# Performance work log

Hardware: AMD Instinct MI355X
Metric: run time of the kernel (lower is better)

Reference implementation:

```python
import jax, jax.numpy as jnp
import numpy as np

B, C, H, W = 4, 256, 128, 256
NUM_CODES = 256  # codebook rows; dim_code == C


def setup_inputs() -> dict:
    key = jax.random.key(0)
    k_feat, k_code = jax.random.split(key)
    feature = jax.random.normal(k_feat, (B, C, H, W), dtype=jnp.float32)
    codebook = jax.random.normal(k_code, (NUM_CODES, C), dtype=jnp.float32)
    return {"feature": feature, "codebook": codebook}


def reference(feature, codebook):
    # Faithful to ComminPub.sender core:
    #   weights = (feature_expand * codebooks).sum(dim=2) / (codebooks*codebooks).sum(dim=2)
    # expressed as a contraction over C instead of materializing [B,N,C,H,W].
    code_norm = jnp.sum(codebook * codebook, axis=1)          # [N]
    weights = jnp.einsum('bchw,nc->bnhw', feature, codebook)   # [B,N,H,W]
    weights = weights / code_norm[None, :, None, None]
    # fc_after_rbdc reconstruction: einsum('b n h w, n c -> b c h w', weights, codebook)
    recon = jnp.einsum('bnhw,nc->bchw', weights, codebook)     # [B,C,H,W]
    return recon
```

## Files before the change

### kernel.cpp

```cpp
#include <hip/hip_runtime.h>
#include <hip/hip_bf16.h>
#include <cstdint>

#define CDIM   256
#define NCODES 256
#define HWB    32768
#define BATCH  4
#define BN     64
#define BK     32

typedef __bf16 bf16x8 __attribute__((ext_vector_type(8)));
typedef float  f32x4  __attribute__((ext_vector_type(4)));

__global__ void norms_kernel(const float* __restrict__ cb, float* __restrict__ inv_norm) {
    const int n = blockIdx.x;
    const int lane = threadIdx.x;
    const float* row = cb + n * CDIM;
    float s = 0.f;
#pragma unroll
    for (int c = 0; c < CDIM; c += 64) {
        float v = row[c + lane];
        s += v * v;
    }
#pragma unroll
    for (int off = 32; off > 0; off >>= 1) s += __shfl_down(s, off, 64);
    if (lane == 0) inv_norm[n] = 1.0f / s;
}

__global__ void mmat_kernel(const float* __restrict__ cb, const float* __restrict__ inv_norm,
                            __bf16* __restrict__ Mb) {
    const int i = blockIdx.x;
    const int j = threadIdx.x;
    float acc = 0.f;
#pragma unroll 4
    for (int n = 0; n < NCODES; ++n) {
        acc += (cb[n * CDIM + i] * inv_norm[n]) * cb[n * CDIM + j];
    }
    Mb[i * CDIM + j] = (__bf16)acc;
}

__global__ __launch_bounds__(256, 4) void recon_kernel(
    const float* __restrict__ feat, const __bf16* __restrict__ Mb,
    float* __restrict__ out) {
    __shared__ __align__(16) __bf16 Alds[CDIM * BK];
    __shared__ __align__(16) __bf16 Blds[BN * BK];

    const int tid  = threadIdx.x;
    const int lane = tid & 63;
    const int w    = tid >> 6;
    const int quad = lane >> 4;
    const int l16  = lane & 15;

    const int b  = blockIdx.y;
    const int p0 = blockIdx.x * BN;

    const float* fbase = feat + ((size_t)b * CDIM) * HWB + p0;
    float*       obase = out  + ((size_t)b * CDIM) * HWB + p0;

    f32x4 acc[4][4];
#pragma unroll
    for (int mt = 0; mt < 4; ++mt)
#pragma unroll
        for (int nt = 0; nt < 4; ++nt)
            acc[mt][nt] = (f32x4){0.f, 0.f, 0.f, 0.f};

    const float* fp = fbase + (size_t)(w * 8) * HWB + lane;

    for (int kc = 0; kc < 8; ++kc) {
        float fv[8];
#pragma unroll
        for (int j = 0; j < 8; ++j)
            fv[j] = fp[(size_t)j * HWB];

#pragma unroll
        for (int j = 0; j < 4; ++j) {
            const int gbase = j * 256 + (w << 6);
            const int g = gbase + lane;
            const __bf16* gsrc = Mb + (g >> 2) * CDIM + kc * BK + (g & 3) * 8;
            __builtin_amdgcn_global_load_lds(
                (const __attribute__((address_space(1))) void*)gsrc,
                (__attribute__((address_space(3))) void*)(Alds + (size_t)gbase * 8),
                16, 0, 0);
        }

        bf16x8 pk;
#pragma unroll
        for (int j = 0; j < 8; ++j) pk[j] = (__bf16)fv[j];
        *(bf16x8*)(Blds + lane * BK + w * 8) = pk;

        __syncthreads();

        bf16x8 bfr[4];
#pragma unroll
        for (int nt = 0; nt < 4; ++nt)
            bfr[nt] = *(const bf16x8*)(Blds + (nt * 16 + l16) * BK + quad * 8);
#pragma unroll
        for (int mt = 0; mt < 4; ++mt) {
            bf16x8 af = *(const bf16x8*)(Alds + (w * 64 + mt * 16 + l16) * BK + quad * 8);
#pragma unroll
            for (int nt = 0; nt < 4; ++nt)
                acc[mt][nt] = __builtin_amdgcn_mfma_f32_16x16x32_bf16(
                    af, bfr[nt], acc[mt][nt], 0, 0, 0);
        }
        __syncthreads();
        fp += (size_t)BK * HWB;
    }

#pragma unroll
    for (int mt = 0; mt < 4; ++mt) {
#pragma unroll
        for (int r = 0; r < 4; ++r) {
            const int c = w * 64 + mt * 16 + quad * 4 + r;
            float* orow = obase + (size_t)c * HWB + l16;
#pragma unroll
            for (int nt = 0; nt < 4; ++nt)
                orow[nt * 16] = acc[mt][nt][r];
        }
    }
}

extern "C" void kernel_launch(void* const* d_in, const int* in_sizes, int n_in,
                              void* d_out, int out_size, void* d_ws, size_t ws_size,
                              hipStream_t stream) {
    const float* feat = (const float*)d_in[0];
    const float* cb   = (const float*)d_in[1];
    float* out = (float*)d_out;

    float*  inv_norm = (float*)d_ws;
    __bf16* Mb       = (__bf16*)((char*)d_ws + 1024);

    norms_kernel<<<NCODES, 64, 0, stream>>>(cb, inv_norm);
    mmat_kernel<<<NCODES, CDIM, 0, stream>>>(cb, inv_norm, Mb);

    dim3 grid(HWB / BN, BATCH);
    recon_kernel<<<grid, 256, 0, stream>>>(feat, Mb, out);
}
```

Measured before the change: 271.6 us.

## Drop LDS staging in recon kernel, register double-buffer loads; fuse prep kernels

The recon kernel no longer stages the feature tile and the projection matrix in LDS. Each lane now loads its MFMA fragments straight from global memory into registers, double-buffered across K chunks, which removes both __syncthreads per iteration. The norm and M-matrix kernels are merged into one prep kernel, saving a launch. In exchange, feature loads become 16-lane strided accesses with less coalescing, register pressure rises (occupancy hint lowered from 4 to 2), and every wave re-reads M from global/L2.

```diff
diff --git a/kernel.cpp b/kernel.cpp
--- a/kernel.cpp
+++ b/kernel.cpp
@@ -7,44 +7,41 @@
 #define HWB    32768
 #define BATCH  4
 #define BN     64
-#define BK     32
 
 typedef __bf16 bf16x8 __attribute__((ext_vector_type(8)));
 typedef float  f32x4  __attribute__((ext_vector_type(4)));
 
-__global__ void norms_kernel(const float* __restrict__ cb, float* __restrict__ inv_norm) {
-    const int n = blockIdx.x;
-    const int lane = threadIdx.x;
-    const float* row = cb + n * CDIM;
-    float s = 0.f;
+__global__ __launch_bounds__(256) void prep_kernel(
+    const float* __restrict__ cb, __bf16* __restrict__ Mb) {
+    __shared__ float g[NCODES];
+    const int i    = blockIdx.x;
+    const int tid  = threadIdx.x;
+    const int lane = tid & 63;
+    const int w    = tid >> 6;
+
+#pragma unroll 4
+    for (int r = 0; r < 64; ++r) {
+        const int n = w * 64 + r;
+        const float* row = cb + n * CDIM;
+        float v0 = row[lane], v1 = row[lane + 64],
+              v2 = row[lane + 128], v3 = row[lane + 192];
+        float s = v0 * v0 + v1 * v1 + v2 * v2 + v3 * v3;
 #pragma unroll
-    for (int c = 0; c < CDIM; c += 64) {
-        float v = row[c + lane];
-        s += v * v;
+        for (int off = 32; off > 0; off >>= 1) s += __shfl_down(s, off, 64);
+        if (lane == 0) g[n] = cb[n * CDIM + i] / s;
     }
-#pragma unroll
-    for (int off = 32; off > 0; off >>= 1) s += __shfl_down(s, off, 64);
-    if (lane == 0) inv_norm[n] = 1.0f / s;
+    __syncthreads();
+
+    float acc = 0.f;
+#pragma unroll 8
+    for (int n = 0; n < NCODES; ++n)
+        acc += g[n] * cb[n * CDIM + tid];
+    Mb[i * CDIM + tid] = (__bf16)acc;
 }
 
-__global__ void mmat_kernel(const float* __restrict__ cb, const float* __restrict__ inv_norm,
-                            __bf16* __restrict__ Mb) {
-    const int i = blockIdx.x;
-    const int j = threadIdx.x;
-    float acc = 0.f;
-#pragma unroll 4
-    for (int n = 0; n < NCODES; ++n) {
-        acc += (cb[n * CDIM + i] * inv_norm[n]) * cb[n * CDIM + j];
-    }
-    Mb[i * CDIM + j] = (__bf16)acc;
-}
-
-__global__ __launch_bounds__(256, 4) void recon_kernel(
+__global__ __launch_bounds__(256, 2) void recon_kernel(
     const float* __restrict__ feat, const __bf16* __restrict__ Mb,
     float* __restrict__ out) {
-    __shared__ __align__(16) __bf16 Alds[CDIM * BK];
-    __shared__ __align__(16) __bf16 Blds[BN * BK];
-
     const int tid  = threadIdx.x;
     const int lane = tid & 63;
     const int w    = tid >> 6;
@@ -54,8 +51,17 @@
     const int b  = blockIdx.y;
     const int p0 = blockIdx.x * BN;
 
-    const float* fbase = feat + ((size_t)b * CDIM) * HWB + p0;
+    const float* fbase = feat + ((size_t)b * CDIM) * HWB + p0 + l16;
     float*       obase = out  + ((size_t)b * CDIM) * HWB + p0;
+
+    const float* fptr[8];
+#pragma unroll
+    for (int j = 0; j < 8; ++j) fptr[j] = fbase + (size_t)(quad * 8 + j) * HWB;
+
+    const __bf16* aptr[4];
+#pragma unroll
+    for (int mt = 0; mt < 4; ++mt)
+        aptr[mt] = Mb + ((w * 64 + mt * 16 + l16) * CDIM + quad * 8);
 
     f32x4 acc[4][4];
 #pragma unroll
@@ -64,46 +70,50 @@
         for (int nt = 0; nt < 4; ++nt)
             acc[mt][nt] = (f32x4){0.f, 0.f, 0.f, 0.f};
 
-    const float* fp = fbase + (size_t)(w * 8) * HWB + lane;
+    float  fv[2][4][8];
+    bf16x8 af[2][4];
 
-    for (int kc = 0; kc < 8; ++kc) {
-        float fv[8];
+#pragma unroll
+    for (int mt = 0; mt < 4; ++mt) af[0][mt] = *(const bf16x8*)(aptr[mt]);
+#pragma unroll
+    for (int nt = 0; nt < 4; ++nt)
 #pragma unroll
         for (int j = 0; j < 8; ++j)
-            fv[j] = fp[(size_t)j * HWB];
+            fv[0][nt][j] = fptr[j][nt * 16];
+#pragma unroll
+    for (int j = 0; j < 8; ++j) fptr[j] += (size_t)32 * HWB;
 
 #pragma unroll
-        for (int j = 0; j < 4; ++j) {
-            const int gbase = j * 256 + (w << 6);
-            const int g = gbase + lane;
-            const __bf16* gsrc = Mb + (g >> 2) * CDIM + kc * BK + (g & 3) * 8;
-            __builtin_amdgcn_global_load_lds(
-                (const __attribute__((address_space(1))) void*)gsrc,
-                (__attribute__((address_space(3))) void*)(Alds + (size_t)gbase * 8),
-                16, 0, 0);
+    for (int kc = 0; kc < 8; ++kc) {
+        const int cur = kc & 1, nxt = cur ^ 1;
+
+        if (kc < 7) {
+#pragma unroll
+            for (int mt = 0; mt < 4; ++mt)
+                af[nxt][mt] = *(const bf16x8*)(aptr[mt] + (kc + 1) * 32);
+#pragma unroll
+            for (int nt = 0; nt < 4; ++nt)
+#pragma unroll
+                for (int j = 0; j < 8; ++j)
+                    fv[nxt][nt][j] = fptr[j][nt * 16];
+#pragma unroll
+            for (int j = 0; j < 8; ++j) fptr[j] += (size_t)32 * HWB;
         }
-
-        bf16x8 pk;
-#pragma unroll
-        for (int j = 0; j < 8; ++j) pk[j] = (__bf16)fv[j];
-        *(bf16x8*)(Blds + lane * BK + w * 8) = pk;
-
-        __syncthreads();
 
         bf16x8 bfr[4];
 #pragma unroll
-        for (int nt = 0; nt < 4; ++nt)
-            bfr[nt] = *(const bf16x8*)(Blds + (nt * 16 + l16) * BK + quad * 8);
+        for (int nt = 0; nt < 4; ++nt) {
+            bf16x8 t;
 #pragma unroll
-        for (int mt = 0; mt < 4; ++mt) {
-            bf16x8 af = *(const bf16x8*)(Alds + (w * 64 + mt * 16 + l16) * BK + quad * 8);
+            for (int j = 0; j < 8; ++j) t[j] = (__bf16)fv[cur][nt][j];
+            bfr[nt] = t;
+        }
+#pragma unroll
+        for (int mt = 0; mt < 4; ++mt)
 #pragma unroll
             for (int nt = 0; nt < 4; ++nt)
                 acc[mt][nt] = __builtin_amdgcn_mfma_f32_16x16x32_bf16(
-                    af, bfr[nt], acc[mt][nt], 0, 0, 0);
-        }
-        __syncthreads();
-        fp += (size_t)BK * HWB;
+                    af[cur][mt], bfr[nt], acc[mt][nt], 0, 0, 0);
     }
 
 #pragma unroll
@@ -126,11 +136,9 @@
     const float* cb   = (const float*)d_in[1];
     float* out = (float*)d_out;
 
-    float*  inv_norm = (float*)d_ws;
-    __bf16* Mb       = (__bf16*)((char*)d_ws + 1024);
+    __bf16* Mb = (__bf16*)d_ws;
 
-    norms_kernel<<<NCODES, 64, 0, stream>>>(cb, inv_norm);
-    mmat_kernel<<<NCODES, CDIM, 0, stream>>>(cb, inv_norm, Mb);
+    prep_kernel<<<NCODES, 256, 0, stream>>>(cb, Mb);
 
     dim3 grid(HWB / BN, BATCH);
     recon_kernel<<<grid, 256, 0, stream>>>(feat, Mb, out);
```

Measured after the change: 313.3 us. +15.4%, slower.

## Enlarge recon tile to 256x256 with double-buffered register-staged LDS pipeline

Applied to the files above, without the earlier changes.

Widens the reconstruction GEMM tile from 64 to 256 pixels per block, uses 512 threads arranged as 4x2 waves, and double-buffers the A/B LDS tiles. The next K-stage is prefetched into registers while MFMAs run, which removes one barrier per stage. LDS writes use an XOR swizzle to avoid bank conflicts. The cost is higher register pressure from 32 accumulators per thread plus staging registers, and fewer blocks to fill the grid.

```diff
diff --git a/kernel.cpp b/kernel.cpp
--- a/kernel.cpp
+++ b/kernel.cpp
@@ -6,11 +6,18 @@
 #define NCODES 256
 #define HWB    32768
 #define BATCH  4
-#define BN     64
+#define BM     256
+#define BN     256
 #define BK     32
+#define NKC    8
 
 typedef __bf16 bf16x8 __attribute__((ext_vector_type(8)));
 typedef float  f32x4  __attribute__((ext_vector_type(4)));
+
+__device__ __forceinline__ unsigned short bfbits(float f) {
+    __bf16 h = (__bf16)f;
+    return *(unsigned short*)&h;
+}
 
 __global__ void norms_kernel(const float* __restrict__ cb, float* __restrict__ inv_norm) {
     const int n = blockIdx.x;
@@ -39,81 +46,117 @@
     Mb[i * CDIM + j] = (__bf16)acc;
 }
 
-__global__ __launch_bounds__(256, 4) void recon_kernel(
+__global__ __launch_bounds__(512, 2) void recon_kernel(
     const float* __restrict__ feat, const __bf16* __restrict__ Mb,
     float* __restrict__ out) {
-    __shared__ __align__(16) __bf16 Alds[CDIM * BK];
-    __shared__ __align__(16) __bf16 Blds[BN * BK];
+    __shared__ __align__(16) unsigned short Abuf[2][BM * BK];
+    __shared__ __align__(16) unsigned short Bbuf[2][BN * BK];
 
     const int tid  = threadIdx.x;
     const int lane = tid & 63;
     const int w    = tid >> 6;
     const int quad = lane >> 4;
     const int l16  = lane & 15;
+    const int wrow = w >> 1;
+    const int wcol = w & 1;
 
+    const int p0 = blockIdx.x * BN;
     const int b  = blockIdx.y;
-    const int p0 = blockIdx.x * BN;
 
     const float* fbase = feat + ((size_t)b * CDIM) * HWB + p0;
     float*       obase = out  + ((size_t)b * CDIM) * HWB + p0;
 
-    f32x4 acc[4][4];
+    const int sp  = tid & 255;
+    const int sg  = tid >> 8;
+    const int swz = (sp >> 1) & 3;
+
+    const unsigned short* asrc = (const unsigned short*)Mb + sp * CDIM + sg * 16;
+    const float* bsrc = fbase + sp;
+
+    uint4 areg[2];
+    float breg[16];
+
+    auto load_stage = [&](int s) {
+        const unsigned short* a = asrc + s * BK;
+        areg[0] = *(const uint4*)(a);
+        areg[1] = *(const uint4*)(a + 8);
+        const size_t krow0 = (size_t)(s * BK + sg * 16) * HWB;
+#pragma unroll
+        for (int kk = 0; kk < 16; ++kk)
+            breg[kk] = bsrc[krow0 + (size_t)kk * HWB];
+    };
+
+    auto write_stage = [&](int buf) {
+        char* Ad = (char*)&Abuf[buf][0];
+        const int o0 = (sg * 2 + 0) ^ swz;
+        const int o1 = (sg * 2 + 1) ^ swz;
+        *(uint4*)(Ad + sp * 64 + o0 * 16) = areg[0];
+        *(uint4*)(Ad + sp * 64 + o1 * 16) = areg[1];
+
+        char* Bd = (char*)&Bbuf[buf][0];
+#pragma unroll
+        for (int j = 0; j < 4; ++j) {
+            const int k  = sg * 16 + j * 4;
+            const int oo = (k >> 3) ^ swz;
+            const int h  = (k >> 2) & 1;
+            uint2 v;
+            v.x = (unsigned)bfbits(breg[j * 4 + 0]) |
+                  ((unsigned)bfbits(breg[j * 4 + 1]) << 16);
+            v.y = (unsigned)bfbits(breg[j * 4 + 2]) |
+                  ((unsigned)bfbits(breg[j * 4 + 3]) << 16);
+            *(uint2*)(Bd + sp * 64 + oo * 16 + h * 8) = v;
+        }
+    };
+
+    f32x4 acc[4][8];
 #pragma unroll
     for (int mt = 0; mt < 4; ++mt)
 #pragma unroll
-        for (int nt = 0; nt < 4; ++nt)
+        for (int nt = 0; nt < 8; ++nt)
             acc[mt][nt] = (f32x4){0.f, 0.f, 0.f, 0.f};
 
-    const float* fp = fbase + (size_t)(w * 8) * HWB + lane;
+    load_stage(0);
+    write_stage(0);
 
-    for (int kc = 0; kc < 8; ++kc) {
-        float fv[8];
+    for (int s = 0; s < NKC; ++s) {
+        __syncthreads();
+        const int buf = s & 1;
+
+        if (s < NKC - 1) load_stage(s + 1);
+
+        bf16x8 af[4];
 #pragma unroll
-        for (int j = 0; j < 8; ++j)
-            fv[j] = fp[(size_t)j * HWB];
+        for (int mt = 0; mt < 4; ++mt) {
+            const int r = wrow * 64 + mt * 16 + l16;
+            af[mt] = *(const bf16x8*)((const char*)&Abuf[buf][0] +
+                                      r * 64 + ((quad ^ ((r >> 1) & 3)) * 16));
+        }
+        bf16x8 bfr[8];
+#pragma unroll
+        for (int nt = 0; nt < 8; ++nt) {
+            const int p = wcol * 128 + nt * 16 + l16;
+            bfr[nt] = *(const bf16x8*)((const char*)&Bbuf[buf][0] +
+                                       p * 64 + ((quad ^ ((p >> 1) & 3)) * 16));
+        }
 
 #pragma unroll
-        for (int j = 0; j < 4; ++j) {
-            const int gbase = j * 256 + (w << 6);
-            const int g = gbase + lane;
-            const __bf16* gsrc = Mb + (g >> 2) * CDIM + kc * BK + (g & 3) * 8;
-            __builtin_amdgcn_global_load_lds(
-                (const __attribute__((address_space(1))) void*)gsrc,
-                (__attribute__((address_space(3))) void*)(Alds + (size_t)gbase * 8),
-                16, 0, 0);
-        }
+        for (int mt = 0; mt < 4; ++mt)
+#pragma unroll
+            for (int nt = 0; nt < 8; ++nt)
+                acc[mt][nt] = __builtin_amdgcn_mfma_f32_16x16x32_bf16(
+                    af[mt], bfr[nt], acc[mt][nt], 0, 0, 0);
 
-        bf16x8 pk;
-#pragma unroll
-        for (int j = 0; j < 8; ++j) pk[j] = (__bf16)fv[j];
-        *(bf16x8*)(Blds + lane * BK + w * 8) = pk;
-
-        __syncthreads();
-
-        bf16x8 bfr[4];
-#pragma unroll
-        for (int nt = 0; nt < 4; ++nt)
-            bfr[nt] = *(const bf16x8*)(Blds + (nt * 16 + l16) * BK + quad * 8);
-#pragma unroll
-        for (int mt = 0; mt < 4; ++mt) {
-            bf16x8 af = *(const bf16x8*)(Alds + (w * 64 + mt * 16 + l16) * BK + quad * 8);
-#pragma unroll
-            for (int nt = 0; nt < 4; ++nt)
-                acc[mt][nt] = __builtin_amdgcn_mfma_f32_16x16x32_bf16(
-                    af, bfr[nt], acc[mt][nt], 0, 0, 0);
-        }
-        __syncthreads();
-        fp += (size_t)BK * HWB;
+        if (s < NKC - 1) write_stage(buf ^ 1);
     }
 
 #pragma unroll
     for (int mt = 0; mt < 4; ++mt) {
 #pragma unroll
         for (int r = 0; r < 4; ++r) {
-            const int c = w * 64 + mt * 16 + quad * 4 + r;
-            float* orow = obase + (size_t)c * HWB + l16;
+            const int c = wrow * 64 + mt * 16 + quad * 4 + r;
+            float* orow = obase + (size_t)c * HWB + wcol * 128 + l16;
 #pragma unroll
-            for (int nt = 0; nt < 4; ++nt)
+            for (int nt = 0; nt < 8; ++nt)
                 orow[nt * 16] = acc[mt][nt][r];
         }
     }
@@ -133,5 +176,5 @@
     mmat_kernel<<<NCODES, CDIM, 0, stream>>>(cb, inv_norm, Mb);
 
     dim3 grid(HWB / BN, BATCH);
-    recon_kernel<<<grid, 256, 0, stream>>>(feat, Mb, out);
+    recon_kernel<<<grid, 512, 0, stream>>>(feat, Mb, out);
 }
```

After: 279.2 us. +2.8%, slower.
